# Optimization experiments

Hardware: AMD Instinct MI355X
Metric: run time of the kernel (lower is better)

Reference implementation:

```python
import jax, jax.numpy as jnp
import numpy as np

EPS = 1e-5
NUM_HEADS = 8
KEY_DIM = 16
D = 64  # attn_ratio * key_dim


def conv1x1_bn(x, w, g, b, m, v):
    # x: (B, Cin, H, W), w: (Cout, Cin); eval-mode BatchNorm over channel dim
    y = jnp.einsum('bchw,oc->bohw', x, w)
    scale = (g * jax.lax.rsqrt(v + EPS))[None, :, None, None]
    shift = (b - g * m * jax.lax.rsqrt(v + EPS))[None, :, None, None]
    return y * scale + shift


def setup_inputs() -> dict:
    key = jax.random.key(0)
    ks = jax.random.split(key, 22)
    dim, nh_kd, dh = 384, 128, 512
    f = jax.random.normal
    u = jax.random.uniform
    return {
        'x': f(ks[0], (2, dim, 56, 56), jnp.float32),
        'wq': f(ks[1], (nh_kd, dim), jnp.float32) * 0.05,
        'qg': u(ks[2], (nh_kd,), jnp.float32), 'qb': f(ks[3], (nh_kd,)) * 0.1,
        'qm': f(ks[4], (nh_kd,)) * 0.1, 'qv': u(ks[5], (nh_kd,)) + 0.5,
        'wk': f(ks[6], (nh_kd, dim), jnp.float32) * 0.05,
        'kg': u(ks[7], (nh_kd,), jnp.float32), 'kb': f(ks[8], (nh_kd,)) * 0.1,
        'km': f(ks[9], (nh_kd,)) * 0.1, 'kvv': u(ks[10], (nh_kd,)) + 0.5,
        'wv': f(ks[11], (dh, dim), jnp.float32) * 0.05,
        'vg': u(ks[12], (dh,), jnp.float32), 'vb': f(ks[13], (dh,)) * 0.1,
        'vm': f(ks[14], (dh,)) * 0.1, 'vvv': u(ks[15], (dh,)) + 0.5,
        'wp': f(ks[16], (dim, dh), jnp.float32) * 0.05,
        'pg': u(ks[17], (dim,), jnp.float32), 'pb': f(ks[18], (dim,)) * 0.1,
        'pm': f(ks[19], (dim,)) * 0.1, 'pvv': u(ks[20], (dim,)) + 0.5,
    }


def reference(x, wq, qg, qb, qm, qv, wk, kg, kb, km, kvv,
              wv, vg, vb, vm, vvv, wp, pg, pb, pm, pvv):
    B, C, H, W = x.shape
    N = H * W
    h, kd, d = NUM_HEADS, KEY_DIM, D
    # (B, h, N, kd)
    qq = conv1x1_bn(x, wq, qg, qb, qm, qv).reshape(B, h, kd, N).transpose(0, 1, 3, 2)
    # (B, h, kd, N)
    kk = conv1x1_bn(x, wk, kg, kb, km, kvv).reshape(B, h, kd, N)
    # (B, h, N, d)
    vv = conv1x1_bn(x, wv, vg, vb, vm, vvv).reshape(B, h, d, N).transpose(0, 1, 3, 2)
    # NOTE: original forward does NOT apply self.scale
    attn = jax.nn.softmax(jnp.matmul(qq, kk), axis=-1)  # (B, h, N, N)
    xx = jnp.matmul(attn, vv)                            # (B, h, N, d)
    xx = xx.transpose(0, 1, 3, 2).reshape(B, h * d, H, W)
    xx = jax.nn.relu(xx)
    return conv1x1_bn(xx, wp, pg, pb, pm, pvv)
```

## Files before the change

### kernel.cpp

```cpp
#include <hip/hip_runtime.h>
#include <hip/hip_bf16.h>

#define B_   2
#define CIN  384
#define NPIX 3136
#define NH   8
#define KD   16
#define DHEAD 64
#define NHKD 128
#define DHD  512
#define EPSW 1e-5f

typedef __attribute__((ext_vector_type(8))) short vshort8;
typedef __attribute__((ext_vector_type(4))) short vshort4;
typedef __attribute__((ext_vector_type(4))) float vfloat4;

static __device__ __forceinline__ float bf2f(short s) {
    unsigned int u = ((unsigned int)(unsigned short)s) << 16;
    return __builtin_bit_cast(float, u);
}
static __device__ __forceinline__ short f2bf(float f) {
    unsigned int u = __builtin_bit_cast(unsigned int, f);
    unsigned int lsb = (u >> 16) & 1u;
    u += 0x7fffu + lsb;
    return (short)(u >> 16);
}
static __device__ __forceinline__ float pget(const void* p, int i, int f32) {
    return f32 ? ((const float*)p)[i] : bf2f(((const short*)p)[i]);
}

__global__ void detect_dtype(const unsigned short* __restrict__ x, int* __restrict__ flag) {
    if (threadIdx.x == 0 && blockIdx.x == 0) {
        int big = 0;
        for (int i = 0; i < 512; i += 2) {
            int e = (x[i] >> 7) & 0xFF;
            if (e >= 0xC0) big++;
        }
        *flag = (big >= 8) ? 1 : 0;
    }
}

__global__ __launch_bounds__(256) void convert_weights(
    const void* __restrict__ wq, const void* __restrict__ wk,
    const void* __restrict__ wv, const void* __restrict__ wp,
    short* __restrict__ wB, const int* __restrict__ flag)
{
    int f32 = *flag;
    int i = blockIdx.x * 256 + threadIdx.x;
    const void* src; int j;
    if (i < 49152)       { src = wq; j = i; }
    else if (i < 98304)  { src = wk; j = i - 49152; }
    else if (i < 294912) { src = wv; j = i - 98304; }
    else                 { src = wp; j = i - 294912; }
    wB[i] = f32 ? f2bf(((const float*)src)[j]) : ((const short*)src)[j];
}

__global__ __launch_bounds__(256) void transpose_k(const void* __restrict__ x,
                                                   short* __restrict__ xT,
                                                   const int* __restrict__ flag) {
    __shared__ short tile[32][33];
    int f32 = *flag;
    int b = blockIdx.z, n0 = blockIdx.x * 32, c0 = blockIdx.y * 32;
    int t = threadIdx.x;
    int r = t >> 3, q4 = (t & 7) * 4;
    size_t off = ((size_t)b * CIN + c0 + r) * NPIX + n0 + q4;
    if (f32) {
        float4 v = *(const float4*)((const float*)x + off);
        tile[r][q4 + 0] = f2bf(v.x);
        tile[r][q4 + 1] = f2bf(v.y);
        tile[r][q4 + 2] = f2bf(v.z);
        tile[r][q4 + 3] = f2bf(v.w);
    } else {
        vshort4 v = *(const vshort4*)((const short*)x + off);
#pragma unroll
        for (int i = 0; i < 4; i++) tile[r][q4 + i] = v[i];
    }
    __syncthreads();
    vshort4 o;
#pragma unroll
    for (int i = 0; i < 4; i++) o[i] = tile[q4 + i][r];
    *(vshort4*)(xT + ((size_t)b * NPIX + n0 + r) * CIN + c0 + q4) = o;
}

__global__ __launch_bounds__(256) void gemm_bt_bn(
    const short* __restrict__ A, long sAb,
    const short* __restrict__ Bt, long sBb,
    void* __restrict__ C, long sCb,
    const void* __restrict__ g, const void* __restrict__ bb,
    const void* __restrict__ mn, const void* __restrict__ vr,
    int Ma, int Nb, int K, int bnPerRow, int finalOut,
    const int* __restrict__ flag)
{
    __shared__ __attribute__((aligned(16))) short Al[64 * 72];
    __shared__ __attribute__((aligned(16))) short Bl[64 * 72];
    int f32 = *flag;
    int b = blockIdx.z;
    const short* Ab = A + (size_t)b * sAb;
    const short* Bb = Bt + (size_t)b * sBb;
    size_t cbase = (size_t)b * sCb;
    int m0 = blockIdx.x * 64, n0 = blockIdx.y * 64;
    int t = threadIdx.x, lane = t & 63, w = t >> 6, m = lane & 15, quad = lane >> 4;
    int srow = t >> 2, scol = (t & 3) * 16;
    const short* ag = Ab + (size_t)(m0 + srow) * K + scol;
    const short* bg = Bb + (size_t)(n0 + srow) * K + scol;
    vfloat4 acc[4];
#pragma unroll
    for (int i = 0; i < 4; i++) acc[i] = (vfloat4){0.f, 0.f, 0.f, 0.f};

    for (int k0 = 0; k0 < K; k0 += 64) {
        vshort8 a0 = *(const vshort8*)(ag + k0);
        vshort8 a1 = *(const vshort8*)(ag + k0 + 8);
        vshort8 b0 = *(const vshort8*)(bg + k0);
        vshort8 b1 = *(const vshort8*)(bg + k0 + 8);
        __syncthreads();
        *(vshort8*)&Al[srow * 72 + scol] = a0;
        *(vshort8*)&Al[srow * 72 + scol + 8] = a1;
        *(vshort8*)&Bl[srow * 72 + scol] = b0;
        *(vshort8*)&Bl[srow * 72 + scol + 8] = b1;
        __syncthreads();
#pragma unroll
        for (int kk = 0; kk < 2; kk++) {
            vshort8 af = *(const vshort8*)&Al[(w * 16 + m) * 72 + kk * 32 + quad * 8];
#pragma unroll
            for (int nc = 0; nc < 4; nc++) {
                vshort8 bf = *(const vshort8*)&Bl[(nc * 16 + m) * 72 + kk * 32 + quad * 8];
                acc[nc] = __builtin_amdgcn_mfma_f32_16x16x32_bf16(af, bf, acc[nc], 0, 0, 0);
            }
        }
    }

#pragma unroll
    for (int nc = 0; nc < 4; nc++) {
#pragma unroll
        for (int r = 0; r < 4; r++) {
            int row = m0 + w * 16 + quad * 4 + r;
            int col = n0 + nc * 16 + m;
            int ch = bnPerRow ? row : col;
            float iv = rsqrtf(pget(vr, ch, f32) + EPSW);
            float sc = pget(g, ch, f32) * iv;
            float sh = pget(bb, ch, f32) - pget(mn, ch, f32) * sc;
            float val = sc * acc[nc][r] + sh;
            size_t idx = cbase + (size_t)row * Nb + col;
            if (finalOut && f32) ((float*)C)[idx] = val;
            else                 ((short*)C)[idx] = f2bf(val);
        }
    }
}

__global__ __launch_bounds__(256) void attn_kernel(
    const short* __restrict__ Qt, const short* __restrict__ Kt,
    const short* __restrict__ V, short* __restrict__ xx)
{
    __shared__ __attribute__((aligned(16))) short Kl[64 * 40];
    __shared__ __attribute__((aligned(16))) short Vl[64 * 72];
    __shared__ __attribute__((aligned(16))) short Pl[64 * 72];
    __shared__ float Ls[64];
    int bh = blockIdx.y, b = bh >> 3, h = bh & 7;
    int q0 = blockIdx.x * 64;
    int t = threadIdx.x, lane = t & 63, w = t >> 6, m = lane & 15, quad = lane >> 4;

    {
        int key = t >> 2;
        int z = 16 + (t & 3) * 4;
        *(vshort4*)&Kl[key * 40 + z] = (vshort4){0, 0, 0, 0};
    }

    int q = q0 + w * 16 + m;
    vshort8 aq;
    if (quad < 2) {
        aq = *(const vshort8*)(Qt + ((size_t)b * NPIX + q) * NHKD + h * KD + quad * 8);
    } else {
        aq = (vshort8){0, 0, 0, 0, 0, 0, 0, 0};
    }

    vfloat4 o[4];
#pragma unroll
    for (int i = 0; i < 4; i++) o[i] = (vfloat4){0.f, 0.f, 0.f, 0.f};
    float Lr = 0.f;

    int skey = t >> 2, skd = (t & 3) * 4;
    const short* kgp = Kt + ((size_t)b * NPIX) * NHKD + h * KD + skd;
    int vrow = t >> 2, vcol = (t & 3) * 16;
    const short* vgp = V + ((size_t)(b * DHD) + h * DHEAD + vrow) * NPIX + vcol;
    const vfloat4 zero4 = (vfloat4){0.f, 0.f, 0.f, 0.f};

    for (int k0 = 0; k0 < NPIX; k0 += 64) {
        vshort4 kstg = *(const vshort4*)(kgp + (size_t)(k0 + skey) * NHKD);
        vshort8 v0 = *(const vshort8*)(vgp + k0);
        vshort8 v1 = *(const vshort8*)(vgp + k0 + 8);
        __syncthreads();
        *(vshort4*)&Kl[skey * 40 + skd] = kstg;
        *(vshort8*)&Vl[vrow * 72 + vcol] = v0;
        *(vshort8*)&Vl[vrow * 72 + vcol + 8] = v1;
        __syncthreads();

        vfloat4 s[4];
#pragma unroll
        for (int c = 0; c < 4; c++) {
            vshort8 ak = *(const vshort8*)&Kl[(c * 16 + m) * 40 + quad * 8];
            s[c] = __builtin_amdgcn_mfma_f32_16x16x32_bf16(ak, aq, zero4, 0, 0, 0);
        }

        short* pw = &Pl[(w * 16 + m) * 72];
#pragma unroll
        for (int c = 0; c < 4; c++) {
            vshort4 pv;
#pragma unroll
            for (int r = 0; r < 4; r++) {
                float p = __expf(s[c][r]);
                Lr += p;
                pv[r] = f2bf(p);
            }
            *(vshort4*)&pw[c * 16 + quad * 4] = pv;
        }

#pragma unroll
        for (int kc = 0; kc < 2; kc++) {
            vshort8 ap = *(const vshort8*)&Pl[(w * 16 + m) * 72 + kc * 32 + quad * 8];
#pragma unroll
            for (int dc = 0; dc < 4; dc++) {
                vshort8 bv = *(const vshort8*)&Vl[(dc * 16 + m) * 72 + kc * 32 + quad * 8];
                o[dc] = __builtin_amdgcn_mfma_f32_16x16x32_bf16(ap, bv, o[dc], 0, 0, 0);
            }
        }
    }

    Lr += __shfl_xor(Lr, 16);
    Lr += __shfl_xor(Lr, 32);
    Ls[w * 16 + m] = Lr;
    __syncthreads();

#pragma unroll
    for (int r = 0; r < 4; r++) {
        float inv = 1.0f / Ls[w * 16 + quad * 4 + r];
        int qrow = q0 + w * 16 + quad * 4 + r;
        size_t base = ((size_t)b * NPIX + qrow) * DHD + h * DHEAD + m;
#pragma unroll
        for (int dc = 0; dc < 4; dc++) {
            float val = o[dc][r] * inv;
            val = fmaxf(val, 0.0f);
            xx[base + dc * 16] = f2bf(val);
        }
    }
}

extern "C" void kernel_launch(void* const* d_in, const int* in_sizes, int n_in,
                              void* d_out, int out_size, void* d_ws, size_t ws_size,
                              hipStream_t stream) {
    const void* x  = d_in[0];
    const void* wq = d_in[1];
    const void* qg = d_in[2];  const void* qb = d_in[3];
    const void* qm = d_in[4];  const void* qv = d_in[5];
    const void* wk = d_in[6];
    const void* kg = d_in[7];  const void* kb = d_in[8];
    const void* km = d_in[9];  const void* kv = d_in[10];
    const void* wv = d_in[11];
    const void* vg = d_in[12]; const void* vb = d_in[13];
    const void* vm = d_in[14]; const void* vv = d_in[15];
    const void* wp = d_in[16];
    const void* pg = d_in[17]; const void* pb = d_in[18];
    const void* pm = d_in[19]; const void* pv = d_in[20];

    short* xT  = (short*)d_ws;
    short* wB  = xT + (size_t)B_ * NPIX * CIN;
    short* wqB = wB;
    short* wkB = wB + 49152;
    short* wvB = wB + 98304;
    short* wpB = wB + 294912;
    short* Qt  = wB + 491520;
    short* Kt  = Qt + (size_t)B_ * NPIX * NHKD;
    short* Vb  = Kt + (size_t)B_ * NPIX * NHKD;
    short* xx  = Vb + (size_t)B_ * DHD * NPIX;
    int* flag  = (int*)(xx + (size_t)B_ * NPIX * DHD);

    detect_dtype<<<1, 64, 0, stream>>>((const unsigned short*)x, flag);
    convert_weights<<<491520 / 256, 256, 0, stream>>>(wq, wk, wv, wp, wB, flag);
    transpose_k<<<dim3(NPIX / 32, CIN / 32, B_), 256, 0, stream>>>(x, xT, flag);

    gemm_bt_bn<<<dim3(NPIX / 64, NHKD / 64, B_), 256, 0, stream>>>(
        xT, (long)NPIX * CIN, wqB, 0, Qt, (long)NPIX * NHKD,
        qg, qb, qm, qv, NPIX, NHKD, CIN, 0, 0, flag);
    gemm_bt_bn<<<dim3(NPIX / 64, NHKD / 64, B_), 256, 0, stream>>>(
        xT, (long)NPIX * CIN, wkB, 0, Kt, (long)NPIX * NHKD,
        kg, kb, km, kv, NPIX, NHKD, CIN, 0, 0, flag);
    gemm_bt_bn<<<dim3(DHD / 64, NPIX / 64, B_), 256, 0, stream>>>(
        wvB, 0, xT, (long)NPIX * CIN, Vb, (long)DHD * NPIX,
        vg, vb, vm, vv, DHD, NPIX, CIN, 1, 0, flag);

    attn_kernel<<<dim3(NPIX / 64, B_ * NH), 256, 0, stream>>>(Qt, Kt, Vb, xx);

    gemm_bt_bn<<<dim3(CIN / 64, NPIX / 64, B_), 256, 0, stream>>>(
        wpB, 0, xx, (long)NPIX * DHD, d_out, (long)CIN * NPIX,
        pg, pb, pm, pv, CIN, NPIX, DHD, 1, 1, flag);
}
```

Before: 236.3 us.

## Use 128x128 GEMM tiles with direct-to-LDS loads, fused Q/K projection and precomputed BN

Replaces the 64x64 GEMM with a 128x128 tile kernel in which each wave computes a 64x64 sub-tile. Tiles are staged through global_load_lds directly into shared memory. Q and K projections are merged into one GEMM writing an interleaved 256-wide buffer, and the pixel dimension is padded to 3200 with bounds-checked stores. BatchNorm scale and shift are precomputed once in a small kernel instead of being recomputed per output element. The aim is better data reuse and fewer launches and epilogue loads, at the cost of higher register pressure, unpadded LDS rows that may cause bank conflicts, and fewer blocks for occupancy.

```diff
diff --git a/kernel.cpp b/kernel.cpp
--- a/kernel.cpp
+++ b/kernel.cpp
@@ -4,10 +4,12 @@
 #define B_   2
 #define CIN  384
 #define NPIX 3136
+#define XPAD 3200
 #define NH   8
 #define KD   16
 #define DHEAD 64
 #define NHKD 128
+#define QKW  256
 #define DHD  512
 #define EPSW 1e-5f
 
@@ -28,6 +30,10 @@
 static __device__ __forceinline__ float pget(const void* p, int i, int f32) {
     return f32 ? ((const float*)p)[i] : bf2f(((const short*)p)[i]);
 }
+
+#define GLOAD16(gp, lp) __builtin_amdgcn_global_load_lds( \
+    (const __attribute__((address_space(1))) void*)(gp),  \
+    (__attribute__((address_space(3))) void*)(lp), 16, 0, 0)
 
 __global__ void detect_dtype(const unsigned short* __restrict__ x, int* __restrict__ flag) {
     if (threadIdx.x == 0 && blockIdx.x == 0) {
@@ -53,6 +59,27 @@
     else if (i < 294912) { src = wv; j = i - 98304; }
     else                 { src = wp; j = i - 294912; }
     wB[i] = f32 ? f2bf(((const float*)src)[j]) : ((const short*)src)[j];
+}
+
+__global__ __launch_bounds__(256) void bn_prep(
+    const void* qg, const void* qb, const void* qm, const void* qv,
+    const void* kg, const void* kb, const void* km, const void* kv,
+    const void* vg, const void* vb, const void* vm, const void* vv,
+    const void* pg, const void* pb, const void* pm, const void* pv,
+    float* __restrict__ scA, float* __restrict__ shA, const int* __restrict__ flag)
+{
+    int f32 = *flag;
+    int i = blockIdx.x * 256 + threadIdx.x;
+    if (i >= 1152) return;
+    const void *g, *bb, *mn, *vr; int j;
+    if (i < 128)      { g = qg; bb = qb; mn = qm; vr = qv; j = i; }
+    else if (i < 256) { g = kg; bb = kb; mn = km; vr = kv; j = i - 128; }
+    else if (i < 768) { g = vg; bb = vb; mn = vm; vr = vv; j = i - 256; }
+    else              { g = pg; bb = pb; mn = pm; vr = pv; j = i - 768; }
+    float iv = rsqrtf(pget(vr, j, f32) + EPSW);
+    float s = pget(g, j, f32) * iv;
+    scA[i] = s;
+    shA[i] = pget(bb, j, f32) - pget(mn, j, f32) * s;
 }
 
 __global__ __launch_bounds__(256) void transpose_k(const void* __restrict__ x,
@@ -79,77 +106,91 @@
     vshort4 o;
 #pragma unroll
     for (int i = 0; i < 4; i++) o[i] = tile[q4 + i][r];
-    *(vshort4*)(xT + ((size_t)b * NPIX + n0 + r) * CIN + c0 + q4) = o;
-}
-
-__global__ __launch_bounds__(256) void gemm_bt_bn(
+    *(vshort4*)(xT + ((size_t)b * XPAD + n0 + r) * CIN + c0 + q4) = o;
+}
+
+__global__ __launch_bounds__(256) void gemm128_bt(
     const short* __restrict__ A, long sAb,
     const short* __restrict__ Bt, long sBb,
-    void* __restrict__ C, long sCb,
-    const void* __restrict__ g, const void* __restrict__ bb,
-    const void* __restrict__ mn, const void* __restrict__ vr,
-    int Ma, int Nb, int K, int bnPerRow, int finalOut,
+    void* __restrict__ C, long sCb, int Crs,
+    const float* __restrict__ sc, const float* __restrict__ sh,
+    int Mreal, int Nreal, int K, int bnPerRow, int finalOut,
     const int* __restrict__ flag)
 {
-    __shared__ __attribute__((aligned(16))) short Al[64 * 72];
-    __shared__ __attribute__((aligned(16))) short Bl[64 * 72];
-    int f32 = *flag;
+    __shared__ __attribute__((aligned(16))) short Al[128 * 64];
+    __shared__ __attribute__((aligned(16))) short Bl[128 * 64];
+    int f32 = finalOut ? *flag : 0;
     int b = blockIdx.z;
     const short* Ab = A + (size_t)b * sAb;
     const short* Bb = Bt + (size_t)b * sBb;
+    int m0 = blockIdx.x * 128, n0 = blockIdx.y * 128;
+    int t = threadIdx.x, lane = t & 63, w = t >> 6;
+    int m = lane & 15, quad = lane >> 4;
+    int wr0 = (w >> 1) * 64, wc0 = (w & 1) * 64;
+
+    const short* ag = Ab + (size_t)(m0 + w * 32 + (lane >> 3)) * K + (lane & 7) * 8;
+    const short* bg = Bb + (size_t)(n0 + w * 32 + (lane >> 3)) * K + (lane & 7) * 8;
+    short* al = &Al[(w * 32) * 64];
+    short* bl = &Bl[(w * 32) * 64];
+
+    vfloat4 acc[4][4];
+#pragma unroll
+    for (int i = 0; i < 4; i++)
+#pragma unroll
+        for (int j = 0; j < 4; j++) acc[i][j] = (vfloat4){0.f, 0.f, 0.f, 0.f};
+
+    for (int k0 = 0; k0 < K; k0 += 64) {
+        __syncthreads();
+#pragma unroll
+        for (int i = 0; i < 4; i++) {
+            GLOAD16(ag + k0 + (size_t)(i * 8) * K, al + i * 8 * 64);
+            GLOAD16(bg + k0 + (size_t)(i * 8) * K, bl + i * 8 * 64);
+        }
+        __syncthreads();
+#pragma unroll
+        for (int kk = 0; kk < 2; kk++) {
+            vshort8 af[4], bf[4];
+#pragma unroll
+            for (int i = 0; i < 4; i++)
+                af[i] = *(const vshort8*)&Al[(wr0 + i * 16 + m) * 64 + kk * 32 + quad * 8];
+#pragma unroll
+            for (int j = 0; j < 4; j++)
+                bf[j] = *(const vshort8*)&Bl[(wc0 + j * 16 + m) * 64 + kk * 32 + quad * 8];
+#pragma unroll
+            for (int i = 0; i < 4; i++)
+#pragma unroll
+                for (int j = 0; j < 4; j++)
+                    acc[i][j] = __builtin_amdgcn_mfma_f32_16x16x32_bf16(af[i], bf[j], acc[i][j], 0, 0, 0);
+        }
+    }
+
     size_t cbase = (size_t)b * sCb;
-    int m0 = blockIdx.x * 64, n0 = blockIdx.y * 64;
-    int t = threadIdx.x, lane = t & 63, w = t >> 6, m = lane & 15, quad = lane >> 4;
-    int srow = t >> 2, scol = (t & 3) * 16;
-    const short* ag = Ab + (size_t)(m0 + srow) * K + scol;
-    const short* bg = Bb + (size_t)(n0 + srow) * K + scol;
-    vfloat4 acc[4];
-#pragma unroll
-    for (int i = 0; i < 4; i++) acc[i] = (vfloat4){0.f, 0.f, 0.f, 0.f};
-
-    for (int k0 = 0; k0 < K; k0 += 64) {
-        vshort8 a0 = *(const vshort8*)(ag + k0);
-        vshort8 a1 = *(const vshort8*)(ag + k0 + 8);
-        vshort8 b0 = *(const vshort8*)(bg + k0);
-        vshort8 b1 = *(const vshort8*)(bg + k0 + 8);
-        __syncthreads();
-        *(vshort8*)&Al[srow * 72 + scol] = a0;
-        *(vshort8*)&Al[srow * 72 + scol + 8] = a1;
-        *(vshort8*)&Bl[srow * 72 + scol] = b0;
-        *(vshort8*)&Bl[srow * 72 + scol + 8] = b1;
-        __syncthreads();
-#pragma unroll
-        for (int kk = 0; kk < 2; kk++) {
-            vshort8 af = *(const vshort8*)&Al[(w * 16 + m) * 72 + kk * 32 + quad * 8];
-#pragma unroll
-            for (int nc = 0; nc < 4; nc++) {
-                vshort8 bf = *(const vshort8*)&Bl[(nc * 16 + m) * 72 + kk * 32 + quad * 8];
-                acc[nc] = __builtin_amdgcn_mfma_f32_16x16x32_bf16(af, bf, acc[nc], 0, 0, 0);
+#pragma unroll
+    for (int i = 0; i < 4; i++) {
+#pragma unroll
+        for (int r = 0; r < 4; r++) {
+            int row = m0 + wr0 + i * 16 + quad * 4 + r;
+            if (row >= Mreal) continue;
+            float scr = bnPerRow ? sc[row] : 0.f;
+            float shr = bnPerRow ? sh[row] : 0.f;
+#pragma unroll
+            for (int j = 0; j < 4; j++) {
+                int col = n0 + wc0 + j * 16 + m;
+                if (col >= Nreal) continue;
+                float s2 = bnPerRow ? scr : sc[col];
+                float h2 = bnPerRow ? shr : sh[col];
+                float val = s2 * acc[i][j][r] + h2;
+                size_t idx = cbase + (size_t)row * Crs + col;
+                if (finalOut && f32) ((float*)C)[idx] = val;
+                else                 ((short*)C)[idx] = f2bf(val);
             }
         }
     }
-
-#pragma unroll
-    for (int nc = 0; nc < 4; nc++) {
-#pragma unroll
-        for (int r = 0; r < 4; r++) {
-            int row = m0 + w * 16 + quad * 4 + r;
-            int col = n0 + nc * 16 + m;
-            int ch = bnPerRow ? row : col;
-            float iv = rsqrtf(pget(vr, ch, f32) + EPSW);
-            float sc = pget(g, ch, f32) * iv;
-            float sh = pget(bb, ch, f32) - pget(mn, ch, f32) * sc;
-            float val = sc * acc[nc][r] + sh;
-            size_t idx = cbase + (size_t)row * Nb + col;
-            if (finalOut && f32) ((float*)C)[idx] = val;
-            else                 ((short*)C)[idx] = f2bf(val);
-        }
-    }
 }
 
 __global__ __launch_bounds__(256) void attn_kernel(
-    const short* __restrict__ Qt, const short* __restrict__ Kt,
-    const short* __restrict__ V, short* __restrict__ xx)
+    const short* __restrict__ QKt, const short* __restrict__ V,
+    short* __restrict__ xx)
 {
     __shared__ __attribute__((aligned(16))) short Kl[64 * 40];
     __shared__ __attribute__((aligned(16))) short Vl[64 * 72];
@@ -168,7 +209,7 @@
     int q = q0 + w * 16 + m;
     vshort8 aq;
     if (quad < 2) {
-        aq = *(const vshort8*)(Qt + ((size_t)b * NPIX + q) * NHKD + h * KD + quad * 8);
+        aq = *(const vshort8*)(QKt + ((size_t)b * XPAD + q) * QKW + h * KD + quad * 8);
     } else {
         aq = (vshort8){0, 0, 0, 0, 0, 0, 0, 0};
     }
@@ -179,13 +220,13 @@
     float Lr = 0.f;
 
     int skey = t >> 2, skd = (t & 3) * 4;
-    const short* kgp = Kt + ((size_t)b * NPIX) * NHKD + h * KD + skd;
+    const short* kgp = QKt + (size_t)b * XPAD * QKW + NHKD + h * KD + skd;
     int vrow = t >> 2, vcol = (t & 3) * 16;
     const short* vgp = V + ((size_t)(b * DHD) + h * DHEAD + vrow) * NPIX + vcol;
     const vfloat4 zero4 = (vfloat4){0.f, 0.f, 0.f, 0.f};
 
     for (int k0 = 0; k0 < NPIX; k0 += 64) {
-        vshort4 kstg = *(const vshort4*)(kgp + (size_t)(k0 + skey) * NHKD);
+        vshort4 kstg = *(const vshort4*)(kgp + (size_t)(k0 + skey) * QKW);
         vshort8 v0 = *(const vshort8*)(vgp + k0);
         vshort8 v1 = *(const vshort8*)(vgp + k0 + 8);
         __syncthreads();
@@ -234,7 +275,7 @@
     for (int r = 0; r < 4; r++) {
         float inv = 1.0f / Ls[w * 16 + quad * 4 + r];
         int qrow = q0 + w * 16 + quad * 4 + r;
-        size_t base = ((size_t)b * NPIX + qrow) * DHD + h * DHEAD + m;
+        size_t base = ((size_t)b * XPAD + qrow) * DHD + h * DHEAD + m;
 #pragma unroll
         for (int dc = 0; dc < 4; dc++) {
             float val = o[dc][r] * inv;
@@ -262,34 +303,33 @@
     const void* pm = d_in[19]; const void* pv = d_in[20];
 
     short* xT  = (short*)d_ws;
-    short* wB  = xT + (size_t)B_ * NPIX * CIN;
-    short* wqB = wB;
-    short* wkB = wB + 49152;
-    short* wvB = wB + 98304;
-    short* wpB = wB + 294912;
-    short* Qt  = wB + 491520;
-    short* Kt  = Qt + (size_t)B_ * NPIX * NHKD;
-    short* Vb  = Kt + (size_t)B_ * NPIX * NHKD;
+    short* wB  = xT + (size_t)B_ * XPAD * CIN;
+    short* wqkB = wB;
+    short* wvB  = wB + 98304;
+    short* wpB  = wB + 294912;
+    short* QKt = wB + 491520;
+    short* Vb  = QKt + (size_t)B_ * XPAD * QKW;
     short* xx  = Vb + (size_t)B_ * DHD * NPIX;
-    int* flag  = (int*)(xx + (size_t)B_ * NPIX * DHD);
+    float* scA = (float*)(xx + (size_t)B_ * XPAD * DHD);
+    float* shA = scA + 1152;
+    int* flag  = (int*)(shA + 1152);
 
     detect_dtype<<<1, 64, 0, stream>>>((const unsigned short*)x, flag);
     convert_weights<<<491520 / 256, 256, 0, stream>>>(wq, wk, wv, wp, wB, flag);
+    bn_prep<<<5, 256, 0, stream>>>(qg, qb, qm, qv, kg, kb, km, kv,
+                                   vg, vb, vm, vv, pg, pb, pm, pv, scA, shA, flag);
     transpose_k<<<dim3(NPIX / 32, CIN / 32, B_), 256, 0, stream>>>(x, xT, flag);
 
-    gemm_bt_bn<<<dim3(NPIX / 64, NHKD / 64, B_), 256, 0, stream>>>(
-        xT, (long)NPIX * CIN, wqB, 0, Qt, (long)NPIX * NHKD,
-        qg, qb, qm, qv, NPIX, NHKD, CIN, 0, 0, flag);
-    gemm_bt_bn<<<dim3(NPIX / 64, NHKD / 64, B_), 256, 0, stream>>>(
-        xT, (long)NPIX * CIN, wkB, 0, Kt, (long)NPIX * NHKD,
-        kg, kb, km, kv, NPIX, NHKD, CIN, 0, 0, flag);
-    gemm_bt_bn<<<dim3(DHD / 64, NPIX / 64, B_), 256, 0, stream>>>(
-        wvB, 0, xT, (long)NPIX * CIN, Vb, (long)DHD * NPIX,
-        vg, vb, vm, vv, DHD, NPIX, CIN, 1, 0, flag);
-
-    attn_kernel<<<dim3(NPIX / 64, B_ * NH), 256, 0, stream>>>(Qt, Kt, Vb, xx);
-
-    gemm_bt_bn<<<dim3(CIN / 64, NPIX / 64, B_), 256, 0, stream>>>(
-        wpB, 0, xx, (long)NPIX * DHD, d_out, (long)CIN * NPIX,
-        pg, pb, pm, pv, CIN, NPIX, DHD, 1, 1, flag);
-}
+    gemm128_bt<<<dim3(XPAD / 128, QKW / 128, B_), 256, 0, stream>>>(
+        xT, (long)XPAD * CIN, wqkB, 0, QKt, (long)XPAD * QKW, QKW,
+        scA, shA, NPIX, QKW, CIN, 0, 0, flag);
+    gemm128_bt<<<dim3(DHD / 128, XPAD / 128, B_), 256, 0, stream>>>(
+        wvB, 0, xT, (long)XPAD * CIN, Vb, (long)DHD * NPIX, NPIX,
+        scA + 256, shA + 256, DHD, NPIX, CIN, 1, 0, flag);
+
+    attn_kernel<<<dim3(NPIX / 64, B_ * NH), 256, 0, stream>>>(QKt, Vb, xx);
+
+    gemm128_bt<<<dim3(CIN / 128, XPAD / 128, B_), 256, 0, stream>>>(
+        wpB, 0, xx, (long)XPAD * DHD, d_out, (long)CIN * NPIX, NPIX,
+        scA + 768, shA + 768, CIN, NPIX, DHD, 1, 1, flag);
+}
```

Measured after the change: 260.1 us. 10.1% more time.
